# Performance work log

Hardware: AMD Instinct MI355X
Metric: run time of the kernel (lower is better)

Reference implementation:

```python
import jax, jax.numpy as jnp
import numpy as np

B = 2048          # batch (vmapped samples)
STEPS = 64        # hardcoded scan length in module
H = 64            # hidden_size
W = 128           # width_size
NZ = 32           # noise_size (control_size)
INZ = 32          # initial_noise_size
D = 8             # data_size


def lipswish(x):
    return 0.909 * jax.nn.silu(x)


def _mlp3(x, W0, b0, W1, b1, W2, b2, act, final_act):
    # eqx.nn.MLP with depth=2: in->width, width->width, width->out
    h = act(x @ W0.T + b0)
    h = act(h @ W1.T + b1)
    return final_act(h @ W2.T + b2)


def setup_inputs() -> dict:
    key = jax.random.key(0)
    ks = jax.random.split(key, 32)

    def lin(k, out_d, in_d):
        lim = 1.0 / np.sqrt(in_d)
        kw, kb = jax.random.split(k)
        Wm = jax.random.uniform(kw, (out_d, in_d), minval=-lim, maxval=lim, dtype=jnp.float32)
        bv = jax.random.uniform(kb, (out_d,), minval=-lim, maxval=lim, dtype=jnp.float32)
        return Wm, bv

    Wi0, bi0 = lin(ks[0], W, INZ)
    Wi1, bi1 = lin(ks[1], W, W)
    Wi2, bi2 = lin(ks[2], H, W)

    Wv0, bv0 = lin(ks[3], W, H + 1)
    Wv1, bv1 = lin(ks[4], W, W)
    Wv2, bv2 = lin(ks[5], H, W)
    scale_v = jax.random.uniform(ks[6], (H,), minval=0.9, maxval=1.1, dtype=jnp.float32)

    Wc0, bc0 = lin(ks[7], W, H + 1)
    Wc1, bc1 = lin(ks[8], W, W)
    Wc2, bc2 = lin(ks[9], H * NZ, W)
    scale_c = jax.random.uniform(ks[10], (H, NZ), minval=0.9, maxval=1.1, dtype=jnp.float32)

    Wr, br = lin(ks[11], D, H)

    ts = jnp.arange(STEPS + 1, dtype=jnp.float32)
    init_noise = jax.random.normal(ks[12], (B, INZ), dtype=jnp.float32)
    bm = jax.random.normal(ks[13], (B, STEPS, NZ), dtype=jnp.float32)

    return dict(ts=ts, init_noise=init_noise, bm=bm,
                Wi0=Wi0, bi0=bi0, Wi1=Wi1, bi1=bi1, Wi2=Wi2, bi2=bi2,
                scale_v=scale_v, Wv0=Wv0, bv0=bv0, Wv1=Wv1, bv1=bv1, Wv2=Wv2, bv2=bv2,
                scale_c=scale_c, Wc0=Wc0, bc0=bc0, Wc1=Wc1, bc1=bc1, Wc2=Wc2, bc2=bc2,
                Wr=Wr, br=br)


def reference(ts, init_noise, bm,
              Wi0, bi0, Wi1, bi1, Wi2, bi2,
              scale_v, Wv0, bv0, Wv1, bv1, Wv2, bv2,
              scale_c, Wc0, bc0, Wc1, bc1, Wc2, bc2,
              Wr, br):
    t0 = ts[0]
    dt = jnp.float32(1.0)  # dt0 hardcoded in module
    sqrt_dt = jnp.sqrt(dt)

    # initial MLP (relu hidden, identity final): noise -> y0 [B,H]
    y0 = _mlp3(init_noise, Wi0, bi0, Wi1, bi1, Wi2, bi2, jax.nn.relu, lambda x: x)

    bm_t = jnp.transpose(bm, (1, 0, 2))  # [STEPS, B, NZ]
    idx = jnp.arange(STEPS, dtype=jnp.float32)

    def step(y, xs):
        i, bm_i = xs
        t = t0 + i * dt
        tcol = jnp.broadcast_to(jnp.reshape(t, (1, 1)), (y.shape[0], 1))
        inp = jnp.concatenate([tcol, y], axis=1)  # [B, H+1]
        # drift vector field
        drift = scale_v * _mlp3(inp, Wv0, bv0, Wv1, bv1, Wv2, bv2, lipswish, jnp.tanh)
        # controlled vector field: [B, H, NZ]
        diff = scale_c * _mlp3(inp, Wc0, bc0, Wc1, bc1, Wc2, bc2, lipswish, jnp.tanh).reshape(-1, H, NZ)
        y1 = y + drift * dt + jnp.einsum('bhn,bn->bh', diff, bm_i * sqrt_dt)
        return y1, y1

    _, ys = jax.lax.scan(step, y0, (idx, bm_t), length=STEPS, unroll=8)  # ys [STEPS,B,H]
    out = jnp.einsum('tbh,dh->tbd', ys, Wr) + br  # readout per step
    return jnp.transpose(out, (1, 0, 2))  # [B, STEPS, D]
```

## Files before the change

kernel.cpp:

```cpp
#include <hip/hip_runtime.h>
#include <stdint.h>
#include <stddef.h>


typedef __attribute__((ext_vector_type(8))) short bf16x8;
typedef __attribute__((ext_vector_type(4))) float f32x4;
typedef __attribute__((ext_vector_type(4))) int   i32x4;

#define BB 16
#define NWG 128

#define WS_WI0 0
#define WS_WI1 8192
#define WS_WI2 40960
#define WS_WV0 57344
#define WS_WV1 73728
#define WS_WV2 106496
#define WS_WC0 122880
#define WS_WC1 139264
#define WS_WC2 172032
#define WS_TV0 696320
#define WS_TC0 696832

#define LD_WV0 0
#define LD_WV1 16384
#define LD_WC0 49152
#define LD_WC1 65536
#define LD_YBF 98304
#define LD_H1V 100352
#define LD_H1C 104448
#define LD_H2V 108544
#define LD_H2C 112640
#define LD_Y   116736
#define LD_DB  121088
#define LD_BM  125440
#define LD_BSC 127552
#define LD_BEV 135744
#define LD_BEC 136256
#define LD_BV1 136768
#define LD_BC1 137280
#define LD_BV2 137792
#define LD_SV  138048
#define LD_WR  138304
#define LD_BR  140480
#define LDS_TOTAL 140512

__device__ __forceinline__ short f2bf(float f) {
  uint32_t u = __builtin_bit_cast(uint32_t, f);
  uint32_t r = (u + 0x7fffu + ((u >> 16) & 1u)) >> 16;
  return (short)r;
}
__device__ __forceinline__ float bf2f(short s) {
  uint32_t u = ((uint32_t)(uint16_t)s) << 16;
  return __builtin_bit_cast(float, u);
}
__device__ __forceinline__ float tanh_fast(float x) {
  float e = __builtin_amdgcn_exp2f(x * 2.8853900817779268f);
  return __builtin_fmaf(-2.f, __builtin_amdgcn_rcpf(e + 1.f), 1.f);
}
__device__ __forceinline__ float lipswish(float x) {
  float s = __builtin_amdgcn_rcpf(1.f + __builtin_amdgcn_exp2f(-1.4426950408889634f * x));
  return 0.909f * x * s;
}
__device__ __forceinline__ float red16(float x) {
  int v;
  v = __builtin_amdgcn_update_dpp(0, __builtin_bit_cast(int, x), 0xB1, 0xF, 0xF, true);
  x += __builtin_bit_cast(float, v);
  v = __builtin_amdgcn_update_dpp(0, __builtin_bit_cast(int, x), 0x4E, 0xF, 0xF, true);
  x += __builtin_bit_cast(float, v);
  v = __builtin_amdgcn_update_dpp(0, __builtin_bit_cast(int, x), 0x141, 0xF, 0xF, true);
  x += __builtin_bit_cast(float, v);
  v = __builtin_amdgcn_update_dpp(0, __builtin_bit_cast(int, x), 0x140, 0xF, 0xF, true);
  x += __builtin_bit_cast(float, v);
  return x;
}
__device__ __forceinline__ float red4(float x) {
  int v;
  v = __builtin_amdgcn_update_dpp(0, __builtin_bit_cast(int, x), 0xB1, 0xF, 0xF, true);
  x += __builtin_bit_cast(float, v);
  v = __builtin_amdgcn_update_dpp(0, __builtin_bit_cast(int, x), 0x4E, 0xF, 0xF, true);
  x += __builtin_bit_cast(float, v);
  return x;
}
__device__ __forceinline__ void write_act(char* buf, int m, int k, short v) {
  int addr = ((k >> 5) << 10) + (m + ((k >> 3) & 3) * 16) * 16 + ((k & 7) << 1);
  *(short*)(buf + addr) = v;
}

template<int KF>
__device__ __forceinline__ f32x4 gemm_tile(const char* abase, const char* bbase, int lane) {
  f32x4 acc = {0.f, 0.f, 0.f, 0.f};
#pragma unroll
  for (int k = 0; k < KF; k++) {
    bf16x8 a = *(const bf16x8*)(abase + k * 1024 + lane * 16);
    bf16x8 b = *(const bf16x8*)(bbase + k * 1024 + lane * 16);
    acc = __builtin_amdgcn_mfma_f32_16x16x32_bf16(a, b, acc, 0, 0, 0);
  }
  return acc;
}

__global__ __launch_bounds__(256) void prep_kernel(
    const float* Wi0, const float* Wi1, const float* Wi2,
    const float* Wv0, const float* Wv1, const float* Wv2,
    const float* Wc0, const float* Wc1, const float* Wc2, char* ws) {
  int gid = blockIdx.x * 256 + threadIdx.x;
  if (gid < 680 * 64) {
    int frag = gid >> 6, lane = gid & 63;
    const float* src; int start, KI, srcK, c0;
    if      (frag < 8)   { src = Wi0; start = 0;   KI = 1; srcK = 32;  c0 = 0; }
    else if (frag < 40)  { src = Wi1; start = 8;   KI = 4; srcK = 128; c0 = 0; }
    else if (frag < 56)  { src = Wi2; start = 40;  KI = 4; srcK = 128; c0 = 0; }
    else if (frag < 72)  { src = Wv0; start = 56;  KI = 2; srcK = 65;  c0 = 1; }
    else if (frag < 104) { src = Wv1; start = 72;  KI = 4; srcK = 128; c0 = 0; }
    else if (frag < 120) { src = Wv2; start = 104; KI = 4; srcK = 128; c0 = 0; }
    else if (frag < 136) { src = Wc0; start = 120; KI = 2; srcK = 65;  c0 = 1; }
    else if (frag < 168) { src = Wc1; start = 136; KI = 4; srcK = 128; c0 = 0; }
    else                 { src = Wc2; start = 168; KI = 4; srcK = 128; c0 = 0; }
    int rel = frag - start;
    int nt = rel / KI, ki = rel % KI;
    int n16 = lane & 15, quad = lane >> 4;
    const float* s = src + (nt * 16 + n16) * srcK + c0 + ki * 32 + quad * 8;
    bf16x8 v;
#pragma unroll
    for (int j = 0; j < 8; j++) v[j] = f2bf(s[j]);
    *(bf16x8*)(ws + (size_t)frag * 1024 + lane * 16) = v;
  } else {
    int i = gid - 680 * 64;
    if (i < 128)      ((float*)(ws + WS_TV0))[i] = Wv0[i * 65];
    else if (i < 256) ((float*)(ws + WS_TC0))[i - 128] = Wc0[(i - 128) * 65];
  }
}

__global__ __launch_bounds__(512, 2)
void sde_kernel(
    const float* ts, const float* init_noise, const float* bm,
    const float* bi0, const float* bi1, const float* bi2,
    const float* bv0, const float* bv1, const float* bv2, const float* scale_v,
    const float* bc0, const float* bc1, const float* bc2, const float* scale_c,
    const float* Wr, const float* br,
    const char* ws, float* out) {
  extern __shared__ __align__(16) char lds[];
  const int tid  = threadIdx.x;
  const int lane = tid & 63;
  const int wv   = tid >> 6;
  const int nl   = lane & 15;
  const int quad = lane >> 4;
  const int b0   = blockIdx.x * BB;
  const char* wc2 = ws + WS_WC2 + (size_t)(wv * 16) * 4096;

  bf16x8 vf0 = {}, vf1 = {}, vf2 = {}, vf3 = {};
  if (wv < 4) {
    vf0 = *(const bf16x8*)(ws + WS_WV2 + wv * 4096 +    0 + lane * 16);
    vf1 = *(const bf16x8*)(ws + WS_WV2 + wv * 4096 + 1024 + lane * 16);
    vf2 = *(const bf16x8*)(ws + WS_WV2 + wv * 4096 + 2048 + lane * 16);
    vf3 = *(const bf16x8*)(ws + WS_WV2 + wv * 4096 + 3072 + lane * 16);
  }
  float tvq = 0.f, bbq = 0.f;
  if (tid >= 256) {
    int j = tid - 256;
    if (j < 128) { tvq = ((const float*)(ws + WS_TV0))[j];       bbq = bv0[j]; }
    else         { tvq = ((const float*)(ws + WS_TC0))[j - 128]; bbq = bc0[j - 128]; }
  }

  {
    const i32x4* s0 = (const i32x4*)(ws + WS_WV0);
    const i32x4* s1 = (const i32x4*)(ws + WS_WC0);
    i32x4* d0 = (i32x4*)(lds + LD_WV0);
    i32x4* d1 = (i32x4*)(lds + LD_WC0);
    for (int j = tid; j < 3072; j += 512) { d0[j] = s0[j]; d1[j] = s1[j]; }
  }
  for (int j = tid; j < 2048; j += 512) {
    uint32_t u = (uint32_t)(uint16_t)f2bf(bc2[j]) |
                 ((uint32_t)(uint16_t)f2bf(scale_c[j]) << 16);
    ((uint32_t*)(lds + LD_BSC))[j] = u;
  }
  if (tid < 128)      { ((float*)(lds + LD_BV1))[tid] = bv1[tid];
                        ((float*)(lds + LD_BC1))[tid] = bc1[tid]; }
  else if (tid < 192) { int k = tid - 128; ((float*)(lds + LD_BV2))[k] = bv2[k];
                        ((float*)(lds + LD_SV))[k] = scale_v[k]; }
  else if (tid < 200) { int k = tid - 192; ((float*)(lds + LD_BR))[k] = br[k]; }
  { int dd = tid >> 6, k = tid & 63;
    ((float*)(lds + LD_WR))[dd * 68 + k] = Wr[dd * 64 + k]; }
  { int m = tid >> 5, k = tid & 31;
    write_act(lds + LD_YBF, m, k, f2bf(init_noise[(b0 + m) * 32 + k])); }
  __syncthreads();

  { f32x4 acc = gemm_tile<1>(lds + LD_YBF, ws + WS_WI0 + wv * 1024, lane);
    int col = wv * 16 + nl; float bias = bi0[col];
#pragma unroll
    for (int r = 0; r < 4; r++)
      write_act(lds + LD_H1V, quad * 4 + r, col, f2bf(fmaxf(0.f, acc[r] + bias))); }
  __syncthreads();
  { f32x4 acc = gemm_tile<4>(lds + LD_H1V, ws + WS_WI1 + wv * 4096, lane);
    int col = wv * 16 + nl; float bias = bi1[col];
#pragma unroll
    for (int r = 0; r < 4; r++)
      write_act(lds + LD_H2V, quad * 4 + r, col, f2bf(fmaxf(0.f, acc[r] + bias))); }
  __syncthreads();
  if (wv < 4) {
    f32x4 acc = gemm_tile<4>(lds + LD_H2V, ws + WS_WI2 + wv * 4096, lane);
    int col = wv * 16 + nl; float bias = bi2[col];
#pragma unroll
    for (int r = 0; r < 4; r++)
      ((float*)(lds + LD_Y))[(quad * 4 + r) * 68 + col] = acc[r] + bias;
  }
  __syncthreads();

  const float ts0 = ts[0];
  for (int e = tid; e < 1024; e += 512) {
    int row = e >> 6, k = e & 63;
    write_act(lds + LD_YBF, row, k, f2bf(((float*)(lds + LD_Y))[row * 68 + k]));
  }
  ((float*)(lds + LD_BM))[(tid >> 5) * 33 + (tid & 31)] =
      bm[((size_t)(b0 + (tid >> 5)) * 64 + 0) * 32 + (tid & 31)];
  if (tid >= 256) {
    int j = tid - 256; float v = bbq + ts0 * tvq;
    if (j < 128) ((float*)(lds + LD_BEV))[j] = v;
    else         ((float*)(lds + LD_BEC))[j - 128] = v;
  }
  __syncthreads();

  for (int step = 0; step < 64; step++) {
    float bm_next = 0.f;
    if (step + 1 < 64)
      bm_next = bm[((size_t)(b0 + (tid >> 5)) * 64 + (step + 1)) * 32 + (tid & 31)];
    bf16x8 bE0 = *(const bf16x8*)(wc2 +    0 + lane * 16);
    bf16x8 bE1 = *(const bf16x8*)(wc2 + 1024 + lane * 16);
    bf16x8 bE2 = *(const bf16x8*)(wc2 + 2048 + lane * 16);
    bf16x8 bE3 = *(const bf16x8*)(wc2 + 3072 + lane * 16);
    bf16x8 bO0 = *(const bf16x8*)(wc2 + 4096 +    0 + lane * 16);
    bf16x8 bO1 = *(const bf16x8*)(wc2 + 4096 + 1024 + lane * 16);
    bf16x8 bO2 = *(const bf16x8*)(wc2 + 4096 + 2048 + lane * 16);
    bf16x8 bO3 = *(const bf16x8*)(wc2 + 4096 + 3072 + lane * 16);

    {
      int col = wv * 16 + nl;
      f32x4 av = gemm_tile<2>(lds + LD_YBF, lds + LD_WV0 + wv * 2048, lane);
      f32x4 ac = gemm_tile<2>(lds + LD_YBF, lds + LD_WC0 + wv * 2048, lane);
      float bv = ((float*)(lds + LD_BEV))[col];
      float bc = ((float*)(lds + LD_BEC))[col];
#pragma unroll
      for (int r = 0; r < 4; r++) {
        write_act(lds + LD_H1V, quad * 4 + r, col, f2bf(lipswish(av[r] + bv)));
        write_act(lds + LD_H1C, quad * 4 + r, col, f2bf(lipswish(ac[r] + bc)));
      }
    }
    __syncthreads();
    {
      int col = wv * 16 + nl;
      f32x4 av = gemm_tile<4>(lds + LD_H1V, lds + LD_WV1 + wv * 4096, lane);
      f32x4 ac = gemm_tile<4>(lds + LD_H1C, lds + LD_WC1 + wv * 4096, lane);
      float bv = ((float*)(lds + LD_BV1))[col];
      float bc = ((float*)(lds + LD_BC1))[col];
#pragma unroll
      for (int r = 0; r < 4; r++) {
        write_act(lds + LD_H2V, quad * 4 + r, col, f2bf(lipswish(av[r] + bv)));
        write_act(lds + LD_H2C, quad * 4 + r, col, f2bf(lipswish(ac[r] + bc)));
      }
    }
    __syncthreads();
    if (wv < 4) {
      f32x4 acc = {0.f, 0.f, 0.f, 0.f};
      acc = __builtin_amdgcn_mfma_f32_16x16x32_bf16(
          *(const bf16x8*)(lds + LD_H2V +    0 + lane * 16), vf0, acc, 0, 0, 0);
      acc = __builtin_amdgcn_mfma_f32_16x16x32_bf16(
          *(const bf16x8*)(lds + LD_H2V + 1024 + lane * 16), vf1, acc, 0, 0, 0);
      acc = __builtin_amdgcn_mfma_f32_16x16x32_bf16(
          *(const bf16x8*)(lds + LD_H2V + 2048 + lane * 16), vf2, acc, 0, 0, 0);
      acc = __builtin_amdgcn_mfma_f32_16x16x32_bf16(
          *(const bf16x8*)(lds + LD_H2V + 3072 + lane * 16), vf3, acc, 0, 0, 0);
      int col = wv * 16 + nl;
      float bias = ((float*)(lds + LD_BV2))[col];
      float sv   = ((float*)(lds + LD_SV))[col];
#pragma unroll
      for (int r = 0; r < 4; r++)
        ((float*)(lds + LD_DB))[(quad * 4 + r) * 68 + col] = sv * tanh_fast(acc[r] + bias);
    }
    {
      bf16x8 a0f = *(const bf16x8*)(lds + LD_H2C +    0 + lane * 16);
      bf16x8 a1f = *(const bf16x8*)(lds + LD_H2C + 1024 + lane * 16);
      bf16x8 a2f = *(const bf16x8*)(lds + LD_H2C + 2048 + lane * 16);
      bf16x8 a3f = *(const bf16x8*)(lds + LD_H2C + 3072 + lane * 16);
      const float* bmp = (const float*)(lds + LD_BM);
      float bmr00 = bmp[(quad * 4 + 0) * 33 + nl];
      float bmr01 = bmp[(quad * 4 + 1) * 33 + nl];
      float bmr02 = bmp[(quad * 4 + 2) * 33 + nl];
      float bmr03 = bmp[(quad * 4 + 3) * 33 + nl];
      float bmr10 = bmp[(quad * 4 + 0) * 33 + 16 + nl];
      float bmr11 = bmp[(quad * 4 + 1) * 33 + 16 + nl];
      float bmr12 = bmp[(quad * 4 + 2) * 33 + 16 + nl];
      float bmr13 = bmp[(quad * 4 + 3) * 33 + 16 + nl];
      const uint32_t* bscp = (const uint32_t*)(lds + LD_BSC) + wv * 256 + nl;
      float ps0, ps1, ps2, ps3;

#define DIFF_PAIR(P)                                                          \
      {                                                     \
        f32x4 acc = {0.f, 0.f, 0.f, 0.f};                                     \
        acc = __builtin_amdgcn_mfma_f32_16x16x32_bf16(a0f, bE0, acc, 0, 0, 0);\
        acc = __builtin_amdgcn_mfma_f32_16x16x32_bf16(a1f, bE1, acc, 0, 0, 0);\
        acc = __builtin_amdgcn_mfma_f32_16x16x32_bf16(a2f, bE2, acc, 0, 0, 0);\
        acc = __builtin_amdgcn_mfma_f32_16x16x32_bf16(a3f, bE3, acc, 0, 0, 0);\
        if ((P) < 7) {                                                        \
          bE0 = *(const bf16x8*)(wc2 + (2*(P)+2)*4096 +    0 + lane*16);      \
          bE1 = *(const bf16x8*)(wc2 + (2*(P)+2)*4096 + 1024 + lane*16);      \
          bE2 = *(const bf16x8*)(wc2 + (2*(P)+2)*4096 + 2048 + lane*16);      \
          bE3 = *(const bf16x8*)(wc2 + (2*(P)+2)*4096 + 3072 + lane*16);      \
        }                                                                     \
        uint32_t bsc = bscp[(2*(P))*16];                                      \
        float bc2v = bf2f((short)(bsc & 0xffffu));                            \
        float scv  = bf2f((short)(bsc >> 16));                                \
        ps0 = tanh_fast(acc[0] + bc2v) * scv * bmr00;                         \
        ps1 = tanh_fast(acc[1] + bc2v) * scv * bmr01;                         \
        ps2 = tanh_fast(acc[2] + bc2v) * scv * bmr02;                         \
        ps3 = tanh_fast(acc[3] + bc2v) * scv * bmr03;                         \
      }                                                                       \
      {                                                    \
        f32x4 acc = {0.f, 0.f, 0.f, 0.f};                                     \
        acc = __builtin_amdgcn_mfma_f32_16x16x32_bf16(a0f, bO0, acc, 0, 0, 0);\
        acc = __builtin_amdgcn_mfma_f32_16x16x32_bf16(a1f, bO1, acc, 0, 0, 0);\
        acc = __builtin_amdgcn_mfma_f32_16x16x32_bf16(a2f, bO2, acc, 0, 0, 0);\
        acc = __builtin_amdgcn_mfma_f32_16x16x32_bf16(a3f, bO3, acc, 0, 0, 0);\
        if ((P) < 7) {                                                        \
          bO0 = *(const bf16x8*)(wc2 + (2*(P)+3)*4096 +    0 + lane*16);      \
          bO1 = *(const bf16x8*)(wc2 + (2*(P)+3)*4096 + 1024 + lane*16);      \
          bO2 = *(const bf16x8*)(wc2 + (2*(P)+3)*4096 + 2048 + lane*16);      \
          bO3 = *(const bf16x8*)(wc2 + (2*(P)+3)*4096 + 3072 + lane*16);      \
        }                                                                     \
        uint32_t bsc = bscp[(2*(P)+1)*16];                                    \
        float bc2v = bf2f((short)(bsc & 0xffffu));                            \
        float scv  = bf2f((short)(bsc >> 16));                                \
        ps0 += tanh_fast(acc[0] + bc2v) * scv * bmr10;                        \
        ps1 += tanh_fast(acc[1] + bc2v) * scv * bmr11;                        \
        ps2 += tanh_fast(acc[2] + bc2v) * scv * bmr12;                        \
        ps3 += tanh_fast(acc[3] + bc2v) * scv * bmr13;                        \
        ps0 = red16(ps0); ps1 = red16(ps1); ps2 = red16(ps2); ps3 = red16(ps3);\
        if (nl < 4) {                                                         \
          int row = quad * 4 + nl;                                            \
          float s = (nl == 0) ? ps0 : (nl == 1) ? ps1 : (nl == 2) ? ps2 : ps3;\
          ((float*)(lds + LD_Y))[row * 68 + (wv * 8 + (P))] += s;             \
        }                                                                     \
      }

      DIFF_PAIR(0)
      DIFF_PAIR(1)
      DIFF_PAIR(2)
      DIFF_PAIR(3)
      DIFF_PAIR(4)
      DIFF_PAIR(5)
      DIFF_PAIR(6)
      DIFF_PAIR(7)
#undef DIFF_PAIR
    }
    __syncthreads();
    if (tid < 256) {
      int row = tid >> 4, kb = (tid & 15) * 4;
      f32x4 yv = *(const f32x4*)(lds + LD_Y  + (row * 68 + kb) * 4);
      f32x4 db = *(const f32x4*)(lds + LD_DB + (row * 68 + kb) * 4);
      f32x4 vn = yv + db;
      *(f32x4*)(lds + LD_Y + (row * 68 + kb) * 4) = vn;
      uint32_t p0 = (uint32_t)(uint16_t)f2bf(vn[0]) | ((uint32_t)(uint16_t)f2bf(vn[1]) << 16);
      uint32_t p1 = (uint32_t)(uint16_t)f2bf(vn[2]) | ((uint32_t)(uint16_t)f2bf(vn[3]) << 16);
      uint64_t p64 = (uint64_t)p0 | ((uint64_t)p1 << 32);
      int addr = LD_YBF + ((kb >> 5) << 10) + (row + ((kb >> 3) & 3) * 16) * 16 + ((kb & 7) << 1);
      *(uint64_t*)(lds + addr) = p64;
    } else if (step + 1 < 64) {
      int j = tid - 256; float v = bbq + (ts0 + (float)(step + 1)) * tvq;
      if (j < 128) ((float*)(lds + LD_BEV))[j] = v;
      else         ((float*)(lds + LD_BEC))[j - 128] = v;
    }
    if (step + 1 < 64)
      ((float*)(lds + LD_BM))[(tid >> 5) * 33 + (tid & 31)] = bm_next;
    __syncthreads();
    {
      int row = (wv << 1) + (lane >> 5);
      int dd  = (lane >> 2) & 7;
      int kg  = lane & 3;
      const float* yr = (const float*)(lds + LD_Y) + row * 68;
      const float* wr = (const float*)(lds + LD_WR) + dd * 68;
      float s = 0.f;
#pragma unroll
      for (int i = 0; i < 16; i++) s = fmaf(yr[kg + 4 * i], wr[kg + 4 * i], s);
      s = red4(s);
      if (kg == 0)
        out[(size_t)(b0 + row) * 512 + step * 8 + dd] =
            s + ((const float*)(lds + LD_BR))[dd];
    }
  }
}

extern "C" void kernel_launch(void* const* d_in, const int* in_sizes, int n_in,
                              void* d_out, int out_size, void* d_ws, size_t ws_size,
                              hipStream_t stream) {
  (void)in_sizes; (void)n_in; (void)out_size; (void)ws_size;
  const float* ts         = (const float*)d_in[0];
  const float* init_noise = (const float*)d_in[1];
  const float* bm         = (const float*)d_in[2];
  const float* Wi0 = (const float*)d_in[3];
  const float* bi0 = (const float*)d_in[4];
  const float* Wi1 = (const float*)d_in[5];
  const float* bi1 = (const float*)d_in[6];
  const float* Wi2 = (const float*)d_in[7];
  const float* bi2 = (const float*)d_in[8];
  const float* scale_v = (const float*)d_in[9];
  const float* Wv0 = (const float*)d_in[10];
  const float* bv0 = (const float*)d_in[11];
  const float* Wv1 = (const float*)d_in[12];
  const float* bv1 = (const float*)d_in[13];
  const float* Wv2 = (const float*)d_in[14];
  const float* bv2 = (const float*)d_in[15];
  const float* scale_c = (const float*)d_in[16];
  const float* Wc0 = (const float*)d_in[17];
  const float* bc0 = (const float*)d_in[18];
  const float* Wc1 = (const float*)d_in[19];
  const float* bc1 = (const float*)d_in[20];
  const float* Wc2 = (const float*)d_in[21];
  const float* bc2 = (const float*)d_in[22];
  const float* Wr  = (const float*)d_in[23];
  const float* br  = (const float*)d_in[24];
  char*  ws  = (char*)d_ws;
  float* out = (float*)d_out;

  hipFuncSetAttribute((const void*)sde_kernel,
                      hipFuncAttributeMaxDynamicSharedMemorySize, LDS_TOTAL);

  prep_kernel<<<171, 256, 0, stream>>>(Wi0, Wi1, Wi2, Wv0, Wv1, Wv2, Wc0, Wc1, Wc2, ws);
  sde_kernel<<<NWG, 512, LDS_TOTAL, stream>>>(
      ts, init_noise, bm, bi0, bi1, bi2, bv0, bv1, bv2, scale_v,
      bc0, bc1, bc2, scale_c, Wr, br, ws, out);
}
```

Measured before the change: 520.4 us.

## Split each batch tile's diffusion output across two workgroups with global flag exchange

After: 494.8 us. 1.05x faster.

```diff
diff --git a/kernel.cpp b/kernel.cpp
--- a/kernel.cpp
+++ b/kernel.cpp
@@ -5,10 +5,11 @@
 
 typedef __attribute__((ext_vector_type(8))) short bf16x8;
 typedef __attribute__((ext_vector_type(4))) float f32x4;
+typedef __attribute__((ext_vector_type(2))) float f32x2;
 typedef __attribute__((ext_vector_type(4))) int   i32x4;
 
 #define BB 16
-#define NWG 128
+#define NWG 256
 
 #define WS_WI0 0
 #define WS_WI1 8192
@@ -21,6 +22,8 @@
 #define WS_WC2 172032
 #define WS_TV0 696320
 #define WS_TC0 696832
+#define WS_XCHG 700416
+#define WS_FLAG 2273280
 
 #define LD_WV0 0
 #define LD_WV1 16384
@@ -104,6 +107,7 @@
     const float* Wv0, const float* Wv1, const float* Wv2,
     const float* Wc0, const float* Wc1, const float* Wc2, char* ws) {
   int gid = blockIdx.x * 256 + threadIdx.x;
+  if (gid < 512) ((unsigned*)(ws + WS_FLAG))[gid] = 0;
   if (gid < 680 * 64) {
     int frag = gid >> 6, lane = gid & 63;
     const float* src; int start, KI, srcK, c0;
@@ -138,22 +142,31 @@
     const float* bv0, const float* bv1, const float* bv2, const float* scale_v,
     const float* bc0, const float* bc1, const float* bc2, const float* scale_c,
     const float* Wr, const float* br,
-    const char* ws, float* out) {
+    char* ws, float* out) {
   extern __shared__ __align__(16) char lds[];
   const int tid  = threadIdx.x;
   const int lane = tid & 63;
   const int wv   = tid >> 6;
   const int nl   = lane & 15;
   const int quad = lane >> 4;
-  const int b0   = blockIdx.x * BB;
-  const char* wc2 = ws + WS_WC2 + (size_t)(wv * 16) * 4096;
+  const int bid  = blockIdx.x;
+  const int ro   = (bid >> 3) & 1;
+  const int pid  = ((bid >> 4) << 3) | (bid & 7);
+  const int b0   = pid * BB;
+  const int hbase = ro << 5;
+  const char* wc2 = ws + WS_WC2 + (size_t)(ro * 64 + wv * 8) * 4096;
+  char* xch = ws + WS_XCHG;
+  unsigned* flags = (unsigned*)(ws + WS_FLAG);
+  const int myflag = (pid << 1) | ro;
+  const int paflag = (pid << 1) | (1 - ro);
 
   bf16x8 vf0 = {}, vf1 = {}, vf2 = {}, vf3 = {};
-  if (wv < 4) {
-    vf0 = *(const bf16x8*)(ws + WS_WV2 + wv * 4096 +    0 + lane * 16);
-    vf1 = *(const bf16x8*)(ws + WS_WV2 + wv * 4096 + 1024 + lane * 16);
-    vf2 = *(const bf16x8*)(ws + WS_WV2 + wv * 4096 + 2048 + lane * 16);
-    vf3 = *(const bf16x8*)(ws + WS_WV2 + wv * 4096 + 3072 + lane * 16);
+  if (wv < 2) {
+    const char* vb = ws + WS_WV2 + (size_t)(ro * 2 + wv) * 4096;
+    vf0 = *(const bf16x8*)(vb +    0 + lane * 16);
+    vf1 = *(const bf16x8*)(vb + 1024 + lane * 16);
+    vf2 = *(const bf16x8*)(vb + 2048 + lane * 16);
+    vf3 = *(const bf16x8*)(vb + 3072 + lane * 16);
   }
   float tvq = 0.f, bbq = 0.f;
   if (tid >= 256) {
@@ -221,9 +234,19 @@
   __syncthreads();
 
   for (int step = 0; step < 64; step++) {
-    float bm_next = 0.f;
-    if (step + 1 < 64)
-      bm_next = bm[((size_t)(b0 + (tid >> 5)) * 64 + (step + 1)) * 32 + (tid & 31)];
+    {
+      int col = wv * 16 + nl;
+      f32x4 av = gemm_tile<2>(lds + LD_YBF, lds + LD_WV0 + wv * 2048, lane);
+      f32x4 ac = gemm_tile<2>(lds + LD_YBF, lds + LD_WC0 + wv * 2048, lane);
+      float bv = ((float*)(lds + LD_BEV))[col];
+      float bc = ((float*)(lds + LD_BEC))[col];
+#pragma unroll
+      for (int r = 0; r < 4; r++) {
+        write_act(lds + LD_H1V, quad * 4 + r, col, f2bf(lipswish(av[r] + bv)));
+        write_act(lds + LD_H1C, quad * 4 + r, col, f2bf(lipswish(ac[r] + bc)));
+      }
+    }
+    __syncthreads();
     bf16x8 bE0 = *(const bf16x8*)(wc2 +    0 + lane * 16);
     bf16x8 bE1 = *(const bf16x8*)(wc2 + 1024 + lane * 16);
     bf16x8 bE2 = *(const bf16x8*)(wc2 + 2048 + lane * 16);
@@ -232,20 +255,6 @@
     bf16x8 bO1 = *(const bf16x8*)(wc2 + 4096 + 1024 + lane * 16);
     bf16x8 bO2 = *(const bf16x8*)(wc2 + 4096 + 2048 + lane * 16);
     bf16x8 bO3 = *(const bf16x8*)(wc2 + 4096 + 3072 + lane * 16);
-
-    {
-      int col = wv * 16 + nl;
-      f32x4 av = gemm_tile<2>(lds + LD_YBF, lds + LD_WV0 + wv * 2048, lane);
-      f32x4 ac = gemm_tile<2>(lds + LD_YBF, lds + LD_WC0 + wv * 2048, lane);
-      float bv = ((float*)(lds + LD_BEV))[col];
-      float bc = ((float*)(lds + LD_BEC))[col];
-#pragma unroll
-      for (int r = 0; r < 4; r++) {
-        write_act(lds + LD_H1V, quad * 4 + r, col, f2bf(lipswish(av[r] + bv)));
-        write_act(lds + LD_H1C, quad * 4 + r, col, f2bf(lipswish(ac[r] + bc)));
-      }
-    }
-    __syncthreads();
     {
       int col = wv * 16 + nl;
       f32x4 av = gemm_tile<4>(lds + LD_H1V, lds + LD_WV1 + wv * 4096, lane);
@@ -259,7 +268,10 @@
       }
     }
     __syncthreads();
-    if (wv < 4) {
+    float bm_next = 0.f;
+    if (step + 1 < 64)
+      bm_next = bm[((size_t)(b0 + (tid >> 5)) * 64 + (step + 1)) * 32 + (tid & 31)];
+    if (wv < 2) {
       f32x4 acc = {0.f, 0.f, 0.f, 0.f};
       acc = __builtin_amdgcn_mfma_f32_16x16x32_bf16(
           *(const bf16x8*)(lds + LD_H2V +    0 + lane * 16), vf0, acc, 0, 0, 0);
@@ -269,7 +281,7 @@
           *(const bf16x8*)(lds + LD_H2V + 2048 + lane * 16), vf2, acc, 0, 0, 0);
       acc = __builtin_amdgcn_mfma_f32_16x16x32_bf16(
           *(const bf16x8*)(lds + LD_H2V + 3072 + lane * 16), vf3, acc, 0, 0, 0);
-      int col = wv * 16 + nl;
+      int col = (ro * 2 + wv) * 16 + nl;
       float bias = ((float*)(lds + LD_BV2))[col];
       float sv   = ((float*)(lds + LD_SV))[col];
 #pragma unroll
@@ -290,7 +302,7 @@
       float bmr11 = bmp[(quad * 4 + 1) * 33 + 16 + nl];
       float bmr12 = bmp[(quad * 4 + 2) * 33 + 16 + nl];
       float bmr13 = bmp[(quad * 4 + 3) * 33 + 16 + nl];
-      const uint32_t* bscp = (const uint32_t*)(lds + LD_BSC) + wv * 256 + nl;
+      const uint32_t* bscp = (const uint32_t*)(lds + LD_BSC) + (ro * 64 + wv * 8) * 16 + nl;
       float ps0, ps1, ps2, ps3;
 
 #define DIFF_PAIR(P)                                                          \
@@ -300,7 +312,7 @@
         acc = __builtin_amdgcn_mfma_f32_16x16x32_bf16(a1f, bE1, acc, 0, 0, 0);\
         acc = __builtin_amdgcn_mfma_f32_16x16x32_bf16(a2f, bE2, acc, 0, 0, 0);\
         acc = __builtin_amdgcn_mfma_f32_16x16x32_bf16(a3f, bE3, acc, 0, 0, 0);\
-        if ((P) < 7) {                                                        \
+        if ((P) < 3) {                                                        \
           bE0 = *(const bf16x8*)(wc2 + (2*(P)+2)*4096 +    0 + lane*16);      \
           bE1 = *(const bf16x8*)(wc2 + (2*(P)+2)*4096 + 1024 + lane*16);      \
           bE2 = *(const bf16x8*)(wc2 + (2*(P)+2)*4096 + 2048 + lane*16);      \
@@ -320,7 +332,7 @@
         acc = __builtin_amdgcn_mfma_f32_16x16x32_bf16(a1f, bO1, acc, 0, 0, 0);\
         acc = __builtin_amdgcn_mfma_f32_16x16x32_bf16(a2f, bO2, acc, 0, 0, 0);\
         acc = __builtin_amdgcn_mfma_f32_16x16x32_bf16(a3f, bO3, acc, 0, 0, 0);\
-        if ((P) < 7) {                                                        \
+        if ((P) < 3) {                                                        \
           bO0 = *(const bf16x8*)(wc2 + (2*(P)+3)*4096 +    0 + lane*16);      \
           bO1 = *(const bf16x8*)(wc2 + (2*(P)+3)*4096 + 1024 + lane*16);      \
           bO2 = *(const bf16x8*)(wc2 + (2*(P)+3)*4096 + 2048 + lane*16);      \
@@ -337,7 +349,7 @@
         if (nl < 4) {                                                         \
           int row = quad * 4 + nl;                                            \
           float s = (nl == 0) ? ps0 : (nl == 1) ? ps1 : (nl == 2) ? ps2 : ps3;\
-          ((float*)(lds + LD_Y))[row * 68 + (wv * 8 + (P))] += s;             \
+          ((float*)(lds + LD_Y))[row * 68 + (hbase + (wv << 2) + (P))] += s;  \
         }                                                                     \
       }
 
@@ -345,42 +357,80 @@
       DIFF_PAIR(1)
       DIFF_PAIR(2)
       DIFF_PAIR(3)
-      DIFF_PAIR(4)
-      DIFF_PAIR(5)
-      DIFF_PAIR(6)
-      DIFF_PAIR(7)
 #undef DIFF_PAIR
     }
     __syncthreads();
-    if (tid < 256) {
-      int row = tid >> 4, kb = (tid & 15) * 4;
-      f32x4 yv = *(const f32x4*)(lds + LD_Y  + (row * 68 + kb) * 4);
-      f32x4 db = *(const f32x4*)(lds + LD_DB + (row * 68 + kb) * 4);
+    char* my_slot = xch + (size_t)(((myflag << 1) | (step & 1))) * 3072;
+    const char* pa_slot = xch + (size_t)(((paflag << 1) | (step & 1))) * 3072;
+    if (tid < 128) {
+      int row = tid >> 3, kq = tid & 7;
+      int c0 = hbase + kq * 4;
+      f32x4 yv = *(const f32x4*)(lds + LD_Y  + (row * 68 + c0) * 4);
+      f32x4 db = *(const f32x4*)(lds + LD_DB + (row * 68 + c0) * 4);
       f32x4 vn = yv + db;
-      *(f32x4*)(lds + LD_Y + (row * 68 + kb) * 4) = vn;
+      *(f32x4*)(lds + LD_Y + (row * 68 + c0) * 4) = vn;
       uint32_t p0 = (uint32_t)(uint16_t)f2bf(vn[0]) | ((uint32_t)(uint16_t)f2bf(vn[1]) << 16);
       uint32_t p1 = (uint32_t)(uint16_t)f2bf(vn[2]) | ((uint32_t)(uint16_t)f2bf(vn[3]) << 16);
       uint64_t p64 = (uint64_t)p0 | ((uint64_t)p1 << 32);
-      int addr = LD_YBF + ((kb >> 5) << 10) + (row + ((kb >> 3) & 3) * 16) * 16 + ((kb & 7) << 1);
-      *(uint64_t*)(lds + addr) = p64;
-    } else if (step + 1 < 64) {
+      int inner = (row + (kq >> 1) * 16) * 16 + ((kq & 1) << 3);
+      *(uint64_t*)(lds + LD_YBF + ro * 1024 + inner) = p64;
+      unsigned long long* pbf = (unsigned long long*)(my_slot);
+      unsigned long long* pf  = (unsigned long long*)(my_slot + 1024);
+      __hip_atomic_store(pbf + (inner >> 3), (unsigned long long)p64,
+                         __ATOMIC_RELAXED, __HIP_MEMORY_SCOPE_AGENT);
+      f32x2 lo = {vn[0], vn[1]}, hi = {vn[2], vn[3]};
+      __hip_atomic_store(pf + 2 * tid,     __builtin_bit_cast(unsigned long long, lo),
+                         __ATOMIC_RELAXED, __HIP_MEMORY_SCOPE_AGENT);
+      __hip_atomic_store(pf + 2 * tid + 1, __builtin_bit_cast(unsigned long long, hi),
+                         __ATOMIC_RELAXED, __HIP_MEMORY_SCOPE_AGENT);
+    } else if (tid >= 256 && step + 1 < 64) {
       int j = tid - 256; float v = bbq + (ts0 + (float)(step + 1)) * tvq;
       if (j < 128) ((float*)(lds + LD_BEV))[j] = v;
       else         ((float*)(lds + LD_BEC))[j - 128] = v;
     }
     if (step + 1 < 64)
       ((float*)(lds + LD_BM))[(tid >> 5) * 33 + (tid & 31)] = bm_next;
+    asm volatile("s_waitcnt vmcnt(0)" ::: "memory");
+    __syncthreads();
+    if (tid == 0) {
+      __hip_atomic_store(flags + myflag, (unsigned)(step + 1),
+                         __ATOMIC_RELAXED, __HIP_MEMORY_SCOPE_AGENT);
+      unsigned want = (unsigned)(step + 1);
+      int guard = 0;
+      while (__hip_atomic_load(flags + paflag, __ATOMIC_RELAXED,
+                               __HIP_MEMORY_SCOPE_AGENT) < want) {
+        __builtin_amdgcn_s_sleep(2);
+        if (++guard > (1 << 20)) break;
+      }
+    }
+    __syncthreads();
+    if (tid < 128) {
+      const unsigned long long* qbf = (const unsigned long long*)(pa_slot);
+      const unsigned long long* qf  = (const unsigned long long*)(pa_slot + 1024);
+      unsigned long long v = __hip_atomic_load(qbf + tid, __ATOMIC_RELAXED,
+                                               __HIP_MEMORY_SCOPE_AGENT);
+      *(unsigned long long*)(lds + LD_YBF + (1 - ro) * 1024 + tid * 8) = v;
+      unsigned long long a = __hip_atomic_load(qf + 2 * tid, __ATOMIC_RELAXED,
+                                               __HIP_MEMORY_SCOPE_AGENT);
+      unsigned long long b = __hip_atomic_load(qf + 2 * tid + 1, __ATOMIC_RELAXED,
+                                               __HIP_MEMORY_SCOPE_AGENT);
+      int row = tid >> 3, kq = tid & 7;
+      char* yd = lds + LD_Y + (row * 68 + ((1 - ro) << 5) + kq * 4) * 4;
+      *(unsigned long long*)(yd)     = a;
+      *(unsigned long long*)(yd + 8) = b;
+    }
     __syncthreads();
     {
-      int row = (wv << 1) + (lane >> 5);
-      int dd  = (lane >> 2) & 7;
-      int kg  = lane & 3;
+      int row = ro * 8 + wv;
+      int dd  = lane >> 3;
+      int kg  = lane & 7;
       const float* yr = (const float*)(lds + LD_Y) + row * 68;
       const float* wr = (const float*)(lds + LD_WR) + dd * 68;
       float s = 0.f;
 #pragma unroll
-      for (int i = 0; i < 16; i++) s = fmaf(yr[kg + 4 * i], wr[kg + 4 * i], s);
+      for (int i = 0; i < 8; i++) s = fmaf(yr[kg + 8 * i], wr[kg + 8 * i], s);
       s = red4(s);
+      s += __shfl_xor(s, 4, 64);
       if (kg == 0)
         out[(size_t)(b0 + row) * 512 + step * 8 + dd] =
             s + ((const float*)(lds + LD_BR))[dd];
```
